# Kernel optimization log

Hardware: AMD Instinct MI355X
Metric: run time of the kernel (lower is better)

The kernel has to match this reference:

```python
import jax, jax.numpy as jnp
import numpy as np


def setup_inputs() -> dict:
    key = jax.random.key(0)
    k1, k2, k3, k4, k5 = jax.random.split(key, 5)
    B, S, T = 512, 1024, 32
    emissions = jax.random.normal(k1, (B, S, T), dtype=jnp.float32)
    tags = jax.random.randint(k2, (B, S), 0, T, dtype=jnp.int64)
    mask = jnp.ones((B, S), dtype=jnp.float32)  # all positions valid; mask[:,0]==1 required
    transitions = jax.random.normal(k3, (T, T), dtype=jnp.float32)
    start_transitions = jax.random.normal(k4, (T,), dtype=jnp.float32)
    end_transitions = jax.random.normal(k5, (T,), dtype=jnp.float32)
    return {
        "emissions": emissions,
        "tags": tags,
        "mask": mask,
        "transitions": transitions,
        "start_transitions": start_transitions,
        "end_transitions": end_transitions,
    }


def _compute_score(emissions, tags, mask, transitions, start_transitions, end_transitions):
    # score of the gold path, fully vectorized over time
    # first step
    score = start_transitions[tags[:, 0]]
    score = score + jnp.take_along_axis(emissions[:, 0], tags[:, 0:1], axis=1)[:, 0]
    # steps 1..S-1
    emit = jnp.take_along_axis(emissions[:, 1:], tags[:, 1:, None], axis=2)[..., 0]  # [B,S-1]
    trans = transitions[tags[:, :-1], tags[:, 1:]]                                   # [B,S-1]
    score = score + ((emit + trans) * mask[:, 1:]).sum(axis=1)
    # end transition from the last valid tag
    last_idx = mask.sum(axis=1).astype(jnp.int32) - 1                                # [B]
    last_tags = jnp.take_along_axis(tags, last_idx[:, None].astype(tags.dtype), axis=1)[:, 0]
    score = score + end_transitions[last_tags]
    return score


def _compute_partition(emissions, mask, transitions, start_transitions, end_transitions):
    # forward algorithm: logsumexp scan over time
    alpha0 = start_transitions + emissions[:, 0]  # [B,T]

    def step(alpha, inp):
        e_i, m_i = inp  # e_i: [B,T], m_i: [B]
        # alpha[b,i] + transitions[i,j] + e_i[b,j] -> logsumexp over i
        scores = alpha[:, :, None] + transitions[None, :, :] + e_i[:, None, :]  # [B,T,T]
        next_alpha = jax.nn.logsumexp(scores, axis=1)                            # [B,T]
        m = m_i[:, None]
        alpha = next_alpha * m + alpha * (1.0 - m)
        return alpha, None

    xs = (jnp.swapaxes(emissions[:, 1:], 0, 1), jnp.swapaxes(mask[:, 1:], 0, 1))
    alpha, _ = jax.lax.scan(step, alpha0, xs)
    alpha = alpha + end_transitions
    return jax.nn.logsumexp(alpha, axis=1)  # [B]


def reference(emissions, tags, mask, transitions, start_transitions, end_transitions):
    score = _compute_score(emissions, tags, mask, transitions, start_transitions, end_transitions)
    partition = _compute_partition(emissions, mask, transitions, start_transitions, end_transitions)
    return -(score - partition).sum()
```

## Files before the change

### kernel.cpp

```cpp
#include <hip/hip_runtime.h>


typedef __attribute__((ext_vector_type(8)))  short    short8;
typedef __attribute__((ext_vector_type(16))) float    f32x16;
typedef __attribute__((ext_vector_type(4)))  unsigned uint4v;
typedef __attribute__((ext_vector_type(2)))  unsigned uint2v;

#define S_N 1024
#define T_N 32
#define B_N 512
#define L_CH 64
#define C_CH 16
#define SCALE_MUL 0.0078125f
#define SCALE_LOG 4.852030263919617f

#define WS_FRAG_DW ((size_t)B_N * C_CH * 512)
#define WS_MSUM_OFF (WS_FRAG_DW)
#define WS_SCORE_OFF (WS_FRAG_DW + 512)
#define WS_NAPP_OFF (WS_FRAG_DW + 1024)

#if __has_builtin(__builtin_amdgcn_cvt_pk_bf16_f32)
typedef __attribute__((ext_vector_type(2))) __bf16 bf16x2;
__device__ __forceinline__ unsigned cvtpk(float lo, float hi) {
    return __builtin_bit_cast(unsigned, __builtin_amdgcn_cvt_pk_bf16_f32(lo, hi));
}
#else
__device__ __forceinline__ unsigned cvtpk(float lo, float hi) {
    const unsigned a = __float_as_uint(lo) + 0x8000u;
    const unsigned b = __float_as_uint(hi) + 0x8000u;
    return __builtin_amdgcn_perm(b, a, 0x07060302u);
}
#endif

#if __has_builtin(__builtin_amdgcn_permlane32_swap)
__device__ __forceinline__ void swap32(unsigned& a, unsigned& b) {
    uint2v r = __builtin_amdgcn_permlane32_swap(a, b, false, false);
    a = r[0]; b = r[1];
}
#else
__device__ __forceinline__ void swap32(unsigned& a, unsigned& b) {
    const int h = (threadIdx.x & 63) >> 5;
    const unsigned sa = (unsigned)__shfl_xor((int)a, 32, 64);
    const unsigned sb = (unsigned)__shfl_xor((int)b, 32, 64);
    const unsigned na = h ? sb : a;
    const unsigned nb = h ? b : sa;
    a = na; b = nb;
}
#endif

__device__ __forceinline__ short8 mk8(const unsigned* a) {
    uint4v u = {a[0], a[1], a[2], a[3]};
    return __builtin_bit_cast(short8, u);
}
__device__ __forceinline__ float bflo(unsigned u) { return __uint_as_float(u << 16); }
__device__ __forceinline__ float bfhi(unsigned u) { return __uint_as_float(u & 0xFFFF0000u); }

__global__ __launch_bounds__(256) void crf_chunk(
    const float* __restrict__ em, const int* __restrict__ tags,
    const float* __restrict__ mask, const float* __restrict__ trans,
    const float* __restrict__ startT, unsigned* __restrict__ wsf,
    float* __restrict__ wsflt)
{
    __shared__ float elds[4][L_CH * T_N];
    const int wib  = threadIdx.x >> 6;
    const int lane = threadIdx.x & 63;
    const int n    = lane & 31;
    const int h    = lane >> 5;
    const int wave = blockIdx.x * 4 + wib;
    const int b    = wave >> 4;
    const int c    = wave & (C_CH - 1);

    float* my = elds[wib];
    const float* eb = em + ((size_t)b * S_N + c * L_CH) * T_N;

    #pragma unroll
    for (int q = 0; q < 8; ++q) {
        const int flat = q * 256 + lane * 4;
        float4 v = *(const float4*)(eb + flat);
        v.x = __expf(v.x) * SCALE_MUL;
        v.y = __expf(v.y) * SCALE_MUL;
        v.z = __expf(v.z) * SCALE_MUL;
        v.w = __expf(v.w) * SCALE_MUL;
        *(float4*)(my + flat) = v;
    }

    const int s0 = c * L_CH;
    const float mv_l = mask[b * S_N + s0 + lane];
    unsigned long long mbits = __ballot(mv_l != 0.0f);
    if (c == 0) mbits &= ~1ull;

    {
        const int s  = s0 + lane;
        const int tc = tags[b * S_N + s];
        int tp = __shfl_up(tc, 1, 64);
        float val;
        if (lane == 0) {
            if (c == 0) {
                val = startT[tc] + eb[tc];
            } else {
                tp = tags[b * S_N + s - 1];
                val = mv_l * (em[((size_t)b * S_N + s) * T_N + tc] + trans[tp * 32 + tc]);
            }
        } else {
            val = mv_l * (em[((size_t)b * S_N + s) * T_N + tc] + trans[tp * 32 + tc]);
        }
        float ms = mv_l;
        #pragma unroll
        for (int d = 32; d > 0; d >>= 1) {
            val += __shfl_xor(val, d, 64);
            ms  += __shfl_xor(ms,  d, 64);
        }
        if (lane == 0) {
            atomicAdd(&wsflt[WS_SCORE_OFF + b], val);
            atomicAdd(&wsflt[WS_MSUM_OFF + b], ms);
            wsflt[WS_NAPP_OFF + b * C_CH + c] = (float)__popcll(mbits);
        }
    }

    __syncthreads();

    float etA[16];
    #pragma unroll
    for (int j = 0; j < 8; ++j) {
        etA[j]     = __expf(trans[n * 32 + 8 * h + j]);
        etA[8 + j] = __expf(trans[n * 32 + 16 + 8 * h + j]);
    }

    unsigned bB1[4] = {0u, 0u, 0u, 0u}, bB2[4] = {0u, 0u, 0u, 0u};
    {
        const int j1 = n - 8 * h;
        if (j1 >= 0 && j1 < 8) bB1[j1 >> 1] |= 0x3F80u << (16 * (j1 & 1));
        const int j2 = n - 16 - 8 * h;
        if (j2 >= 0 && j2 < 8) bB2[j2 >> 1] |= 0x3F80u << (16 * (j2 & 1));
    }

    const f32x16 Zacc = {};

    #pragma unroll 8
    for (int r = L_CH - 1; r >= 0; --r) {
        if (!((mbits >> r) & 1ull)) continue;

        const float* er = my + r * 32;
        const float4 e0 = *(const float4*)(er + 8 * h);
        const float4 e1 = *(const float4*)(er + 8 * h + 4);
        const float4 e2 = *(const float4*)(er + 16 + 8 * h);
        const float4 e3 = *(const float4*)(er + 16 + 8 * h + 4);
        unsigned a1[4], a2[4];
        a1[0] = cvtpk(etA[0]  * e0.x, etA[1]  * e0.y);
        a1[1] = cvtpk(etA[2]  * e0.z, etA[3]  * e0.w);
        a1[2] = cvtpk(etA[4]  * e1.x, etA[5]  * e1.y);
        a1[3] = cvtpk(etA[6]  * e1.z, etA[7]  * e1.w);
        a2[0] = cvtpk(etA[8]  * e2.x, etA[9]  * e2.y);
        a2[1] = cvtpk(etA[10] * e2.z, etA[11] * e2.w);
        a2[2] = cvtpk(etA[12] * e3.x, etA[13] * e3.y);
        a2[3] = cvtpk(etA[14] * e3.z, etA[15] * e3.w);

        f32x16 D = __builtin_amdgcn_mfma_f32_32x32x16_bf16(mk8(a1), mk8(bB1), Zacc, 0, 0, 0);
        D        = __builtin_amdgcn_mfma_f32_32x32x16_bf16(mk8(a2), mk8(bB2), D,    0, 0, 0);

        unsigned p0 = cvtpk(D[0],  D[1]);
        unsigned p1 = cvtpk(D[2],  D[3]);
        unsigned p2 = cvtpk(D[4],  D[5]);
        unsigned p3 = cvtpk(D[6],  D[7]);
        unsigned p4 = cvtpk(D[8],  D[9]);
        unsigned p5 = cvtpk(D[10], D[11]);
        unsigned p6 = cvtpk(D[12], D[13]);
        unsigned p7 = cvtpk(D[14], D[15]);
        swap32(p0, p2); swap32(p1, p3); swap32(p4, p6); swap32(p5, p7);
        bB1[0] = p0; bB1[1] = p1; bB1[2] = p2; bB1[3] = p3;
        bB2[0] = p4; bB2[1] = p5; bB2[2] = p6; bB2[3] = p7;
    }

    unsigned* dst = wsf + ((size_t)(b * C_CH + c) * 64 + lane) * 8;
    ((uint4*)dst)[0] = make_uint4(bB1[0], bB1[1], bB1[2], bB1[3]);
    ((uint4*)dst)[1] = make_uint4(bB2[0], bB2[1], bB2[2], bB2[3]);
}

__global__ __launch_bounds__(256) void crf_combine(
    const float* __restrict__ em, const int* __restrict__ tags,
    const float* __restrict__ startT, const float* __restrict__ endT,
    const unsigned* __restrict__ wsf, const float* __restrict__ wsflt,
    float* __restrict__ out)
{
    const int lane = threadIdx.x & 63;
    const int n = lane & 31, h = lane >> 5;
    const int b = blockIdx.x * 4 + (threadIdx.x >> 6);

    float a0 = startT[n] + em[(size_t)b * S_N * T_N + n];
    float m = a0;
    #pragma unroll
    for (int d = 16; d > 0; d >>= 1) m = fmaxf(m, __shfl_xor(m, d, 32));
    float A = __expf(a0 - m);
    float Lacc = m;
    float ntot = 0.0f;

    const uint4* fb = (const uint4*)(wsf + (size_t)b * C_CH * 512);
    uint4 q0 = fb[lane * 2];
    uint4 q1 = fb[lane * 2 + 1];

    for (int c = 0; c < C_CH; ++c) {
        uint4 n0 = q0, n1 = q1;
        if (c + 1 < C_CH) {
            n0 = fb[(c + 1) * 128 + lane * 2];
            n1 = fb[(c + 1) * 128 + lane * 2 + 1];
        }
        ntot += wsflt[WS_NAPP_OFF + b * C_CH + c];

        float part = 0.0f;
        part = fmaf(__shfl(A, 8 * h + 0, 32), bflo(q0.x), part);
        part = fmaf(__shfl(A, 8 * h + 1, 32), bfhi(q0.x), part);
        part = fmaf(__shfl(A, 8 * h + 2, 32), bflo(q0.y), part);
        part = fmaf(__shfl(A, 8 * h + 3, 32), bfhi(q0.y), part);
        part = fmaf(__shfl(A, 8 * h + 4, 32), bflo(q0.z), part);
        part = fmaf(__shfl(A, 8 * h + 5, 32), bfhi(q0.z), part);
        part = fmaf(__shfl(A, 8 * h + 6, 32), bflo(q0.w), part);
        part = fmaf(__shfl(A, 8 * h + 7, 32), bfhi(q0.w), part);
        part = fmaf(__shfl(A, 16 + 8 * h + 0, 32), bflo(q1.x), part);
        part = fmaf(__shfl(A, 16 + 8 * h + 1, 32), bfhi(q1.x), part);
        part = fmaf(__shfl(A, 16 + 8 * h + 2, 32), bflo(q1.y), part);
        part = fmaf(__shfl(A, 16 + 8 * h + 3, 32), bfhi(q1.y), part);
        part = fmaf(__shfl(A, 16 + 8 * h + 4, 32), bflo(q1.z), part);
        part = fmaf(__shfl(A, 16 + 8 * h + 5, 32), bfhi(q1.z), part);
        part = fmaf(__shfl(A, 16 + 8 * h + 6, 32), bflo(q1.w), part);
        part = fmaf(__shfl(A, 16 + 8 * h + 7, 32), bfhi(q1.w), part);
        part += __shfl_xor(part, 32);

        float mm = part;
        #pragma unroll
        for (int d = 16; d > 0; d >>= 1) mm = fmaxf(mm, __shfl_xor(mm, d, 32));
        A = part / mm;
        Lacc += __logf(mm);
        q0 = n0; q1 = n1;
    }

    float v = A * __expf(endT[n]);
    #pragma unroll
    for (int d = 16; d > 0; d >>= 1) v += __shfl_xor(v, d, 32);
    if (lane == 0) {
        const int len = (int)(wsflt[WS_MSUM_OFF + b] + 0.5f);
        const int lt  = tags[b * S_N + len - 1];
        const float res = Lacc + __logf(v) + ntot * SCALE_LOG
                          - endT[lt] - wsflt[WS_SCORE_OFF + b];
        atomicAdd(out, res);
    }
}

extern "C" void kernel_launch(void* const* d_in, const int* in_sizes, int n_in,
                              void* d_out, int out_size, void* d_ws, size_t ws_size,
                              hipStream_t stream) {
    const float* em     = (const float*)d_in[0];
    const int*   tags   = (const int*)  d_in[1];
    const float* mask   = (const float*)d_in[2];
    const float* trans  = (const float*)d_in[3];
    const float* startT = (const float*)d_in[4];
    const float* endT   = (const float*)d_in[5];
    float* out = (float*)d_out;

    unsigned* wsf   = (unsigned*)d_ws;
    float*    wsflt = (float*)d_ws;

    hipMemsetAsync(out, 0, sizeof(float), stream);
    hipMemsetAsync((char*)d_ws + WS_MSUM_OFF * 4, 0, 4096, stream);

    hipLaunchKernelGGL(crf_chunk, dim3(2048), dim3(256), 0, stream,
                       em, tags, mask, trans, startT, wsf, wsflt);
    hipLaunchKernelGGL(crf_combine, dim3(128), dim3(256), 0, stream,
                       em, tags, startT, endT, wsf, wsflt, out);
}
```

Measured before the change: 192.4 us.

## Split chunk products into forward/backward halves and meet in the middle in combine

Chunks in the first half now carry a state vector forward, while chunks in the second half carry one backward from the end. The combine kernel runs two waves per batch row, one walking forward and one backward, and joins them through shared memory, which halves the serial combine chain. Emissions are pre-exponentiated and stored as packed bf16 in a permuted LDS layout, so the transition matrix becomes a loop-invariant MFMA operand and the per-step lane swaps go away. A separate unrolled path handles fully unmasked chunks, at the cost of more code and permutation index logic.

```diff
diff --git a/kernel.cpp b/kernel.cpp
--- a/kernel.cpp
+++ b/kernel.cpp
@@ -4,7 +4,6 @@
 typedef __attribute__((ext_vector_type(8)))  short    short8;
 typedef __attribute__((ext_vector_type(16))) float    f32x16;
 typedef __attribute__((ext_vector_type(4)))  unsigned uint4v;
-typedef __attribute__((ext_vector_type(2)))  unsigned uint2v;
 
 #define S_N 1024
 #define T_N 32
@@ -32,28 +31,13 @@
 }
 #endif
 
-#if __has_builtin(__builtin_amdgcn_permlane32_swap)
-__device__ __forceinline__ void swap32(unsigned& a, unsigned& b) {
-    uint2v r = __builtin_amdgcn_permlane32_swap(a, b, false, false);
-    a = r[0]; b = r[1];
-}
-#else
-__device__ __forceinline__ void swap32(unsigned& a, unsigned& b) {
-    const int h = (threadIdx.x & 63) >> 5;
-    const unsigned sa = (unsigned)__shfl_xor((int)a, 32, 64);
-    const unsigned sb = (unsigned)__shfl_xor((int)b, 32, 64);
-    const unsigned na = h ? sb : a;
-    const unsigned nb = h ? b : sa;
-    a = na; b = nb;
-}
-#endif
-
 __device__ __forceinline__ short8 mk8(const unsigned* a) {
     uint4v u = {a[0], a[1], a[2], a[3]};
     return __builtin_bit_cast(short8, u);
 }
 __device__ __forceinline__ float bflo(unsigned u) { return __uint_as_float(u << 16); }
 __device__ __forceinline__ float bfhi(unsigned u) { return __uint_as_float(u & 0xFFFF0000u); }
+__device__ __forceinline__ int PIx(int x) { return (x & ~12) | ((x & 4) << 1) | ((x & 8) >> 1); }
 
 __global__ __launch_bounds__(256) void crf_chunk(
     const float* __restrict__ em, const int* __restrict__ tags,
@@ -61,7 +45,7 @@
     const float* __restrict__ startT, unsigned* __restrict__ wsf,
     float* __restrict__ wsflt)
 {
-    __shared__ float elds[4][L_CH * T_N];
+    __shared__ unsigned elds[4][L_CH * 16];
     const int wib  = threadIdx.x >> 6;
     const int lane = threadIdx.x & 63;
     const int n    = lane & 31;
@@ -70,18 +54,16 @@
     const int b    = wave >> 4;
     const int c    = wave & (C_CH - 1);
 
-    float* my = elds[wib];
+    unsigned* my = elds[wib];
     const float* eb = em + ((size_t)b * S_N + c * L_CH) * T_N;
 
     #pragma unroll
-    for (int q = 0; q < 8; ++q) {
-        const int flat = q * 256 + lane * 4;
-        float4 v = *(const float4*)(eb + flat);
-        v.x = __expf(v.x) * SCALE_MUL;
-        v.y = __expf(v.y) * SCALE_MUL;
-        v.z = __expf(v.z) * SCALE_MUL;
-        v.w = __expf(v.w) * SCALE_MUL;
-        *(float4*)(my + flat) = v;
+    for (int i = 0; i < 16; ++i) {
+        const int flat = i * 64 + lane;
+        const int r = flat >> 4, m = flat & 15;
+        const int base = ((m & 4) << 2) + ((m & 2) << 2) + ((m & 1) << 1) + ((m >> 3) << 2);
+        const float2 v = *(const float2*)(eb + r * 32 + base);
+        my[r * 16 + m] = cvtpk(__expf(v.x) * SCALE_MUL, __expf(v.y) * SCALE_MUL);
     }
 
     const int s0 = c * L_CH;
@@ -116,77 +98,119 @@
             wsflt[WS_NAPP_OFF + b * C_CH + c] = (float)__popcll(mbits);
         }
     }
-
     __syncthreads();
 
-    float etA[16];
+    const bool fwdDir = (c < 8);
+    const f32x16 Zacc = {};
+
+    unsigned A1[4], A2[4];
     #pragma unroll
-    for (int j = 0; j < 8; ++j) {
-        etA[j]     = __expf(trans[n * 32 + 8 * h + j]);
-        etA[8 + j] = __expf(trans[n * 32 + 16 + 8 * h + j]);
-    }
-
-    unsigned bB1[4] = {0u, 0u, 0u, 0u}, bB2[4] = {0u, 0u, 0u, 0u};
-    {
-        const int j1 = n - 8 * h;
-        if (j1 >= 0 && j1 < 8) bB1[j1 >> 1] |= 0x3F80u << (16 * (j1 & 1));
-        const int j2 = n - 16 - 8 * h;
-        if (j2 >= 0 && j2 < 8) bB2[j2 >> 1] |= 0x3F80u << (16 * (j2 & 1));
-    }
-
-    const f32x16 Zacc = {};
-
-    #pragma unroll 8
-    for (int r = L_CH - 1; r >= 0; --r) {
-        if (!((mbits >> r) & 1ull)) continue;
-
-        const float* er = my + r * 32;
-        const float4 e0 = *(const float4*)(er + 8 * h);
-        const float4 e1 = *(const float4*)(er + 8 * h + 4);
-        const float4 e2 = *(const float4*)(er + 16 + 8 * h);
-        const float4 e3 = *(const float4*)(er + 16 + 8 * h + 4);
-        unsigned a1[4], a2[4];
-        a1[0] = cvtpk(etA[0]  * e0.x, etA[1]  * e0.y);
-        a1[1] = cvtpk(etA[2]  * e0.z, etA[3]  * e0.w);
-        a1[2] = cvtpk(etA[4]  * e1.x, etA[5]  * e1.y);
-        a1[3] = cvtpk(etA[6]  * e1.z, etA[7]  * e1.w);
-        a2[0] = cvtpk(etA[8]  * e2.x, etA[9]  * e2.y);
-        a2[1] = cvtpk(etA[10] * e2.z, etA[11] * e2.w);
-        a2[2] = cvtpk(etA[12] * e3.x, etA[13] * e3.y);
-        a2[3] = cvtpk(etA[14] * e3.z, etA[15] * e3.w);
-
-        f32x16 D = __builtin_amdgcn_mfma_f32_32x32x16_bf16(mk8(a1), mk8(bB1), Zacc, 0, 0, 0);
-        D        = __builtin_amdgcn_mfma_f32_32x32x16_bf16(mk8(a2), mk8(bB2), D,    0, 0, 0);
-
-        unsigned p0 = cvtpk(D[0],  D[1]);
-        unsigned p1 = cvtpk(D[2],  D[3]);
-        unsigned p2 = cvtpk(D[4],  D[5]);
-        unsigned p3 = cvtpk(D[6],  D[7]);
-        unsigned p4 = cvtpk(D[8],  D[9]);
-        unsigned p5 = cvtpk(D[10], D[11]);
-        unsigned p6 = cvtpk(D[12], D[13]);
-        unsigned p7 = cvtpk(D[14], D[15]);
-        swap32(p0, p2); swap32(p1, p3); swap32(p4, p6); swap32(p5, p7);
-        bB1[0] = p0; bB1[1] = p1; bB1[2] = p2; bB1[3] = p3;
-        bB2[0] = p4; bB2[1] = p5; bB2[2] = p6; bB2[3] = p7;
-    }
-
-    unsigned* dst = wsf + ((size_t)(b * C_CH + c) * 64 + lane) * 8;
-    ((uint4*)dst)[0] = make_uint4(bB1[0], bB1[1], bB1[2], bB1[3]);
-    ((uint4*)dst)[1] = make_uint4(bB2[0], bB2[1], bB2[2], bB2[3]);
-}
-
-__global__ __launch_bounds__(256) void crf_combine(
+    for (int j = 0; j < 4; ++j) {
+        const int k1 = PIx(8 * h + 2 * j);
+        const int k2 = PIx(16 + 8 * h + 2 * j);
+        if (fwdDir) {
+            A1[j] = cvtpk(__expf(trans[n * 32 + k1]), __expf(trans[n * 32 + k1 + 1]));
+            A2[j] = cvtpk(__expf(trans[n * 32 + k2]), __expf(trans[n * 32 + k2 + 1]));
+        } else {
+            A1[j] = cvtpk(__expf(trans[k1 * 32 + n]), __expf(trans[(k1 + 1) * 32 + n]));
+            A2[j] = cvtpk(__expf(trans[k2 * 32 + n]), __expf(trans[(k2 + 1) * 32 + n]));
+        }
+    }
+    const short8 A1v = mk8(A1), A2v = mk8(A2);
+    const bool clean = ((mbits | (c == 0 ? 1ull : 0ull)) == ~0ull);
+
+    if (fwdDir) {
+        f32x16 D;
+        #pragma unroll
+        for (int i = 0; i < 16; ++i) {
+            const int row = (i & 3) + 8 * (i >> 2) + 4 * h;
+            D[i] = (row == n) ? 1.0f : 0.0f;
+        }
+        #define STEP_FWD(r_) { \
+            const uint4 su = *(const uint4*)(my + (r_) * 16 + h * 8); \
+            const uint4 sv = *(const uint4*)(my + (r_) * 16 + h * 8 + 4); \
+            unsigned S[8]; \
+            S[0] = cvtpk(D[0]  * bflo(su.x), D[1]  * bfhi(su.x)); \
+            S[1] = cvtpk(D[2]  * bflo(su.y), D[3]  * bfhi(su.y)); \
+            S[2] = cvtpk(D[4]  * bflo(su.z), D[5]  * bfhi(su.z)); \
+            S[3] = cvtpk(D[6]  * bflo(su.w), D[7]  * bfhi(su.w)); \
+            S[4] = cvtpk(D[8]  * bflo(sv.x), D[9]  * bfhi(sv.x)); \
+            S[5] = cvtpk(D[10] * bflo(sv.y), D[11] * bfhi(sv.y)); \
+            S[6] = cvtpk(D[12] * bflo(sv.z), D[13] * bfhi(sv.z)); \
+            S[7] = cvtpk(D[14] * bflo(sv.w), D[15] * bfhi(sv.w)); \
+            f32x16 t_ = __builtin_amdgcn_mfma_f32_32x32x16_bf16(A1v, mk8(&S[0]), Zacc, 0, 0, 0); \
+            D = __builtin_amdgcn_mfma_f32_32x32x16_bf16(A2v, mk8(&S[4]), t_, 0, 0, 0); \
+        }
+        if (clean) {
+            #pragma unroll 4
+            for (int r = 63; r >= 1; --r) STEP_FWD(r);
+            if (c != 0) STEP_FWD(0);
+        } else {
+            for (int r = 63; r >= 0; --r)
+                if ((mbits >> r) & 1ull) STEP_FWD(r);
+        }
+        unsigned* dst = wsf + ((size_t)(b * C_CH + c) * 64 + lane) * 8;
+        ((uint4*)dst)[0] = make_uint4(cvtpk(D[0], D[1]),  cvtpk(D[2], D[3]),
+                                      cvtpk(D[4], D[5]),  cvtpk(D[6], D[7]));
+        ((uint4*)dst)[1] = make_uint4(cvtpk(D[8], D[9]),  cvtpk(D[10], D[11]),
+                                      cvtpk(D[12], D[13]), cvtpk(D[14], D[15]));
+    } else {
+        unsigned S[8] = {0u, 0u, 0u, 0u, 0u, 0u, 0u, 0u};
+        {
+            const int pn = PIx(n);
+            if (((pn >> 3) & 1) == h) {
+                const int j = pn & 7;
+                const unsigned val = 0x3F80u << (16 * (j & 1));
+                if (n < 16) S[j >> 1] |= val; else S[4 + (j >> 1)] |= val;
+            }
+        }
+        #define STEP_BWD(r_) { \
+            f32x16 t_ = __builtin_amdgcn_mfma_f32_32x32x16_bf16(A1v, mk8(&S[0]), Zacc, 0, 0, 0); \
+            t_ = __builtin_amdgcn_mfma_f32_32x32x16_bf16(A2v, mk8(&S[4]), t_, 0, 0, 0); \
+            const uint4 su = *(const uint4*)(my + (r_) * 16 + h * 8); \
+            const uint4 sv = *(const uint4*)(my + (r_) * 16 + h * 8 + 4); \
+            S[0] = cvtpk(t_[0]  * bflo(su.x), t_[1]  * bfhi(su.x)); \
+            S[1] = cvtpk(t_[2]  * bflo(su.y), t_[3]  * bfhi(su.y)); \
+            S[2] = cvtpk(t_[4]  * bflo(su.z), t_[5]  * bfhi(su.z)); \
+            S[3] = cvtpk(t_[6]  * bflo(su.w), t_[7]  * bfhi(su.w)); \
+            S[4] = cvtpk(t_[8]  * bflo(sv.x), t_[9]  * bfhi(sv.x)); \
+            S[5] = cvtpk(t_[10] * bflo(sv.y), t_[11] * bfhi(sv.y)); \
+            S[6] = cvtpk(t_[12] * bflo(sv.z), t_[13] * bfhi(sv.z)); \
+            S[7] = cvtpk(t_[14] * bflo(sv.w), t_[15] * bfhi(sv.w)); \
+        }
+        if (clean) {
+            #pragma unroll 4
+            for (int r = 0; r < 64; ++r) STEP_BWD(r);
+        } else {
+            for (int r = 0; r < 64; ++r)
+                if ((mbits >> r) & 1ull) STEP_BWD(r);
+        }
+        unsigned* dst = wsf + ((size_t)(b * C_CH + c) * 64 + lane) * 8;
+        ((uint4*)dst)[0] = make_uint4(S[0], S[1], S[2], S[3]);
+        ((uint4*)dst)[1] = make_uint4(S[4], S[5], S[6], S[7]);
+    }
+}
+
+__global__ __launch_bounds__(128) void crf_combine(
     const float* __restrict__ em, const int* __restrict__ tags,
     const float* __restrict__ startT, const float* __restrict__ endT,
     const unsigned* __restrict__ wsf, const float* __restrict__ wsflt,
     float* __restrict__ out)
 {
+    __shared__ float sm[68];
     const int lane = threadIdx.x & 63;
+    const int w = threadIdx.x >> 6;
     const int n = lane & 31, h = lane >> 5;
-    const int b = blockIdx.x * 4 + (threadIdx.x >> 6);
-
-    float a0 = startT[n] + em[(size_t)b * S_N * T_N + n];
+    const int b = blockIdx.x;
+
+    int idxA[8], idxB[8];
+    #pragma unroll
+    for (int j = 0; j < 8; ++j) {
+        idxA[j] = PIx(8 * h + j);
+        idxB[j] = PIx(16 + 8 * h + j);
+    }
+
+    float a0 = (w == 0) ? (startT[n] + em[(size_t)b * S_N * T_N + n]) : endT[n];
     float m = a0;
     #pragma unroll
     for (int d = 16; d > 0; d >>= 1) m = fmaxf(m, __shfl_xor(m, d, 32));
@@ -195,34 +219,38 @@
     float ntot = 0.0f;
 
     const uint4* fb = (const uint4*)(wsf + (size_t)b * C_CH * 512);
-    uint4 q0 = fb[lane * 2];
-    uint4 q1 = fb[lane * 2 + 1];
-
-    for (int c = 0; c < C_CH; ++c) {
+    const int c0 = (w == 0) ? 0 : 15;
+    const int dc = (w == 0) ? 1 : -1;
+    uint4 q0 = fb[c0 * 128 + lane * 2];
+    uint4 q1 = fb[c0 * 128 + lane * 2 + 1];
+
+    for (int i = 0; i < 8; ++i) {
+        const int c = c0 + i * dc;
         uint4 n0 = q0, n1 = q1;
-        if (c + 1 < C_CH) {
-            n0 = fb[(c + 1) * 128 + lane * 2];
-            n1 = fb[(c + 1) * 128 + lane * 2 + 1];
+        if (i + 1 < 8) {
+            n0 = fb[(c + dc) * 128 + lane * 2];
+            n1 = fb[(c + dc) * 128 + lane * 2 + 1];
         }
         ntot += wsflt[WS_NAPP_OFF + b * C_CH + c];
 
-        float part = 0.0f;
-        part = fmaf(__shfl(A, 8 * h + 0, 32), bflo(q0.x), part);
-        part = fmaf(__shfl(A, 8 * h + 1, 32), bfhi(q0.x), part);
-        part = fmaf(__shfl(A, 8 * h + 2, 32), bflo(q0.y), part);
-        part = fmaf(__shfl(A, 8 * h + 3, 32), bfhi(q0.y), part);
-        part = fmaf(__shfl(A, 8 * h + 4, 32), bflo(q0.z), part);
-        part = fmaf(__shfl(A, 8 * h + 5, 32), bfhi(q0.z), part);
-        part = fmaf(__shfl(A, 8 * h + 6, 32), bflo(q0.w), part);
-        part = fmaf(__shfl(A, 8 * h + 7, 32), bfhi(q0.w), part);
-        part = fmaf(__shfl(A, 16 + 8 * h + 0, 32), bflo(q1.x), part);
-        part = fmaf(__shfl(A, 16 + 8 * h + 1, 32), bfhi(q1.x), part);
-        part = fmaf(__shfl(A, 16 + 8 * h + 2, 32), bflo(q1.y), part);
-        part = fmaf(__shfl(A, 16 + 8 * h + 3, 32), bfhi(q1.y), part);
-        part = fmaf(__shfl(A, 16 + 8 * h + 4, 32), bflo(q1.z), part);
-        part = fmaf(__shfl(A, 16 + 8 * h + 5, 32), bfhi(q1.z), part);
-        part = fmaf(__shfl(A, 16 + 8 * h + 6, 32), bflo(q1.w), part);
-        part = fmaf(__shfl(A, 16 + 8 * h + 7, 32), bfhi(q1.w), part);
+        float p0 = 0.f, p1 = 0.f, p2 = 0.f, p3 = 0.f;
+        p0 = fmaf(__shfl(A, idxA[0], 32), bflo(q0.x), p0);
+        p1 = fmaf(__shfl(A, idxA[1], 32), bfhi(q0.x), p1);
+        p2 = fmaf(__shfl(A, idxA[2], 32), bflo(q0.y), p2);
+        p3 = fmaf(__shfl(A, idxA[3], 32), bfhi(q0.y), p3);
+        p0 = fmaf(__shfl(A, idxA[4], 32), bflo(q0.z), p0);
+        p1 = fmaf(__shfl(A, idxA[5], 32), bfhi(q0.z), p1);
+        p2 = fmaf(__shfl(A, idxA[6], 32), bflo(q0.w), p2);
+        p3 = fmaf(__shfl(A, idxA[7], 32), bfhi(q0.w), p3);
+        p0 = fmaf(__shfl(A, idxB[0], 32), bflo(q1.x), p0);
+        p1 = fmaf(__shfl(A, idxB[1], 32), bfhi(q1.x), p1);
+        p2 = fmaf(__shfl(A, idxB[2], 32), bflo(q1.y), p2);
+        p3 = fmaf(__shfl(A, idxB[3], 32), bfhi(q1.y), p3);
+        p0 = fmaf(__shfl(A, idxB[4], 32), bflo(q1.z), p0);
+        p1 = fmaf(__shfl(A, idxB[5], 32), bfhi(q1.z), p1);
+        p2 = fmaf(__shfl(A, idxB[6], 32), bflo(q1.w), p2);
+        p3 = fmaf(__shfl(A, idxB[7], 32), bfhi(q1.w), p3);
+        float part = (p0 + p1) + (p2 + p3);
         part += __shfl_xor(part, 32);
 
         float mm = part;
@@ -233,15 +261,20 @@
         q0 = n0; q1 = n1;
     }
 
-    float v = A * __expf(endT[n]);
-    #pragma unroll
-    for (int d = 16; d > 0; d >>= 1) v += __shfl_xor(v, d, 32);
-    if (lane == 0) {
-        const int len = (int)(wsflt[WS_MSUM_OFF + b] + 0.5f);
-        const int lt  = tags[b * S_N + len - 1];
-        const float res = Lacc + __logf(v) + ntot * SCALE_LOG
-                          - endT[lt] - wsflt[WS_SCORE_OFF + b];
-        atomicAdd(out, res);
+    if (h == 0) sm[w * 32 + n] = A;
+    if (lane == 0) { sm[64 + w] = Lacc; sm[66 + w] = ntot; }
+    __syncthreads();
+
+    if (threadIdx.x < 32) {
+        float v = sm[threadIdx.x] * sm[32 + threadIdx.x];
+        #pragma unroll
+        for (int d = 16; d > 0; d >>= 1) v += __shfl_xor(v, d, 32);
+        if (threadIdx.x == 0) {
+            const float part = sm[64] + sm[65] + __logf(v) + (sm[66] + sm[67]) * SCALE_LOG;
+            const int len = (int)(wsflt[WS_MSUM_OFF + b] + 0.5f);
+            const int lt  = tags[b * S_N + len - 1];
+            atomicAdd(out, part - endT[lt] - wsflt[WS_SCORE_OFF + b]);
+        }
     }
 }
 
@@ -264,6 +297,6 @@
 
     hipLaunchKernelGGL(crf_chunk, dim3(2048), dim3(256), 0, stream,
                        em, tags, mask, trans, startT, wsf, wsflt);
-    hipLaunchKernelGGL(crf_combine, dim3(128), dim3(256), 0, stream,
+    hipLaunchKernelGGL(crf_combine, dim3(512), dim3(128), 0, stream,
                        em, tags, startT, endT, wsf, wsflt, out);
 }
```

After: 178.3 us. 7.4% less time.
